# Optimization experiments

Hardware: AMD Instinct MI355X
Metric: run time of the kernel (lower is better)

## Reference

```python
import jax, jax.numpy as jnp
import numpy as np

AX = (-2, -1)
LAMBDA = 0.05
ITERS = 6

# torch fft_2d_img  = fftshift(ifft2(ifftshift(x)))  (used in the FORWARD model)
# torch ifft_2d_img = ifftshift(fft2(fftshift(x)))   (used in the ADJOINT model)

def _fwd_xform(x):
    return jnp.fft.fftshift(jnp.fft.ifft2(jnp.fft.ifftshift(x, axes=AX), axes=AX, norm='ortho'), axes=AX)

def _adj_xform(x):
    return jnp.fft.ifftshift(jnp.fft.fft2(jnp.fft.fftshift(x, axes=AX), axes=AX, norm='ortho'), axes=AX)

def _forward_model(img, S, mask):
    # img [b,t,h,w] -> masked multicoil k-space [b,t,c,h,w]
    return mask * _fwd_xform(S * img[:, :, None])

def _adjoint_model(k, S):
    # k [b,t,c,h,w] -> coil-combined image [b,t,h,w]
    return jnp.sum(jnp.conj(S) * _adj_xform(k), axis=2)

def _system_matrix_R(p, S, L, mask):
    # p [b,sv,h,w]; L [b,t,sv]
    expanded = jnp.einsum('bts,bshw->bthw', L, p)
    combined = _adjoint_model(_forward_model(expanded, S, mask), S)
    out = jnp.einsum('bts,bthw->bshw', jnp.conj(L), combined)
    return out + LAMBDA * p

def _cg_solve(b_vec, S, L, mask):
    z0 = jnp.zeros_like(b_vec)
    rs0 = jnp.vdot(b_vec, b_vec)

    def step(carry, _):
        z, r, p, rs_old, done = carry
        Ap = _system_matrix_R(p, S, L, mask)
        alpha = rs_old / (jnp.vdot(p, Ap) + 1e-20)
        z_n = z + alpha * p
        r_n = r - alpha * Ap
        rs_new = jnp.vdot(r_n, r_n)
        p_n = r_n + (rs_new / (rs_old + 1e-20)) * p
        # replicate torch early-break: freeze state once residual is tiny
        z_o = jnp.where(done, z, z_n)
        r_o = jnp.where(done, r, r_n)
        p_o = jnp.where(done, p, p_n)
        rs_o = jnp.where(done, rs_old, rs_new)
        done_n = done | (jnp.abs(rs_o) < 1e-10)
        return (z_o, r_o, p_o, rs_o, done_n), None

    carry0 = (z0, b_vec, b_vec, rs0, jnp.array(False))
    (z, _, _, _, _), _ = jax.lax.scan(step, carry0, None, length=ITERS)
    return z

def setup_inputs() -> dict:
    key = jax.random.key(0)
    ks = jax.random.split(key, 9)
    b, t, c, h, w, sv = 2, 12, 10, 256, 256, 3
    f32 = jnp.float32
    inp = {
        'k_real': jax.random.normal(ks[0], (b, t, c, h, w), f32),
        'k_imag': jax.random.normal(ks[1], (b, t, c, h, w), f32),
        'mo_real': jax.random.normal(ks[2], (b, sv, h, w), f32),
        'mo_imag': jax.random.normal(ks[3], (b, sv, h, w), f32),
        's_real': jax.random.normal(ks[4], (b, 1, c, h, w), f32),
        's_imag': jax.random.normal(ks[5], (b, 1, c, h, w), f32),
        'tb_real': jax.random.normal(ks[6], (b, t, sv), f32),
        'tb_imag': jax.random.normal(ks[7], (b, t, sv), f32),
        'mask': (jax.random.uniform(ks[8], (b, t, 1, h, w)) < 0.35).astype(f32),
    }
    return inp

def reference(k_real, k_imag, mo_real, mo_imag, s_real, s_imag, tb_real, tb_imag, mask):
    Y = k_real + 1j * k_imag          # [b,t,c,h,w]
    MO = mo_real + 1j * mo_imag       # [b,sv,h,w]
    S = s_real + 1j * s_imag          # [b,1,c,h,w]
    L = tb_real + 1j * tb_imag        # [b,t,sv]
    # b = L^H A^H Y + lambda * model_output
    b_vec = jnp.einsum('bts,bthw->bshw', jnp.conj(L), _adjoint_model(Y, S)) + LAMBDA * MO
    z = _cg_solve(b_vec, S, L, mask)  # [b,sv,h,w] complex
    return jnp.stack([z.real, z.imag], axis=-1)  # [b,sv,h,w,2] float32
```

## Files before the change

kernel.cpp:

```cpp
#include <hip/hip_runtime.h>
#include <math.h>

#define HW 65536
#define LAM 0.05f

struct Scal {
  double pap_re, pap_im, rs_acc, rs_old;
  int done, cnt;
};

__device__ __forceinline__ float2 cadd(float2 a, float2 b){ return make_float2(a.x+b.x, a.y+b.y); }
__device__ __forceinline__ float2 csub(float2 a, float2 b){ return make_float2(a.x-b.x, a.y-b.y); }
__device__ __forceinline__ float2 cmul(float2 a, float2 b){
  return make_float2(a.x*b.x - a.y*b.y, a.x*b.y + a.y*b.x);
}
__device__ __forceinline__ float2 cmulj(float2 a, float2 b){
  return make_float2(a.x*b.x + a.y*b.y, a.x*b.y - a.y*b.x);
}
__device__ __forceinline__ int rev4(int p){
  return ((p&3)<<6) | (((p>>2)&3)<<4) | (((p>>4)&3)<<2) | ((p>>6)&3);
}
__device__ __forceinline__ int swz(int p){ return p ^ (p>>4); }

__device__ __forceinline__ void wave_lds_sync(){
  __builtin_amdgcn_wave_barrier();
  __asm__ __volatile__("s_waitcnt lgkmcnt(0)" ::: "memory");
  __builtin_amdgcn_wave_barrier();
}

template<int SIGN>
__device__ __forceinline__ void bfly4(float2 x0, float2 x1, float2 x2, float2 x3,
                                      float2& y0, float2& y1, float2& y2, float2& y3){
  float2 a  = cadd(x0,x2), bm = csub(x0,x2);
  float2 c  = cadd(x1,x3), d  = csub(x1,x3);
  float2 jd = make_float2(-(float)SIGN*d.y, (float)SIGN*d.x);
  y0 = cadd(a,c); y2 = csub(a,c); y1 = cadd(bm,jd); y3 = csub(bm,jd);
}

template<int SIGN>
__device__ void wave_fft256w_x2(float2* bA, float2* bB, int lane){
#pragma unroll
  for (int st=0; st<4; ++st){
    const int B = 256 >> (2*st);
    const int Q = B >> 2;
    int m   = lane & (Q-1);
    int blk = lane >> (6 - 2*st);
    int p0  = blk*B + m;
    int i0 = swz(p0), i1 = swz(p0+Q), i2 = swz(p0+2*Q), i3 = swz(p0+3*Q);
    float2 xA0=bA[i0], xA1=bA[i1], xA2=bA[i2], xA3=bA[i3];
    float2 xB0=bB[i0], xB1=bB[i1], xB2=bB[i2], xB3=bB[i3];
    float2 yA0,yA1,yA2,yA3, yB0,yB1,yB2,yB3;
    bfly4<SIGN>(xA0,xA1,xA2,xA3, yA0,yA1,yA2,yA3);
    bfly4<SIGN>(xB0,xB1,xB2,xB3, yB0,yB1,yB2,yB3);
    if (st < 3){
      float ang = (float)SIGN * 6.28318530717958647f * (float)m / (float)B;
      float s1, c1;
      __sincosf(ang, &s1, &c1);
      float2 w1 = make_float2(c1, s1);
      float2 w2 = make_float2(c1*c1 - s1*s1, 2.f*c1*s1);
      float2 w3 = cmul(w1, w2);
      bA[i0]=yA0; bA[i1]=cmul(yA1,w1); bA[i2]=cmul(yA2,w2); bA[i3]=cmul(yA3,w3);
      bB[i0]=yB0; bB[i1]=cmul(yB1,w1); bB[i2]=cmul(yB2,w2); bB[i3]=cmul(yB3,w3);
    } else {
      int r0=swz(rev4(4*lane+0)), r1=swz(rev4(4*lane+1));
      int r2=swz(rev4(4*lane+2)), r3=swz(rev4(4*lane+3));
      bA[r0]=yA0; bA[r1]=yA1; bA[r2]=yA2; bA[r3]=yA3;
      bB[r0]=yB0; bB[r1]=yB1; bB[r2]=yB2; bB[r3]=yB3;
    }
    wave_lds_sync();
  }
}

__global__ __launch_bounds__(256) void k_w(const float* __restrict__ mask,
                                           const float* __restrict__ tbr,
                                           const float* __restrict__ tbi,
                                           float2* __restrict__ Wb,
                                           Scal* sc){
  if (blockIdx.x==0 && blockIdx.y==0 && threadIdx.x==0){
    sc->pap_re=0.0; sc->pap_im=0.0; sc->rs_acc=0.0; sc->rs_old=0.0;
    sc->done=0; sc->cnt=0;
  }
  __shared__ float2 wt[9][16][17];
  int tid = threadIdx.x;
  int bx = blockIdx.x;
  int b  = blockIdx.y;
  int u0 = (bx>>4)<<4, v0 = (bx&15)<<4;
  int u_l = tid>>4, v_l = tid&15;
  int pix = (u0+u_l)*256 + (v0+v_l);
  float d0=0,d1=0,d2=0, o01r=0,o01i=0, o02r=0,o02i=0, o12r=0,o12i=0;
#pragma unroll
  for (int t=0;t<12;t++){
    float m = mask[(size_t)(b*12+t)*HW + pix];
    int lb = (b*12+t)*3;
    float l0r = tbr[lb+0], l0i = tbi[lb+0];
    float l1r = tbr[lb+1], l1i = tbi[lb+1];
    float l2r = tbr[lb+2], l2i = tbi[lb+2];
    d0 += m*(l0r*l0r + l0i*l0i);
    d1 += m*(l1r*l1r + l1i*l1i);
    d2 += m*(l2r*l2r + l2i*l2i);
    o01r += m*(l0r*l1r + l0i*l1i); o01i += m*(l0r*l1i - l0i*l1r);
    o02r += m*(l0r*l2r + l0i*l2i); o02i += m*(l0r*l2i - l0i*l2r);
    o12r += m*(l1r*l2r + l1i*l2i); o12i += m*(l1r*l2i - l1i*l2r);
  }
  const float s = 1.0f/65536.0f;
  wt[0][u_l][v_l] = make_float2(d0*s, 0.f);
  wt[1][u_l][v_l] = make_float2(o01r*s,  o01i*s);
  wt[2][u_l][v_l] = make_float2(o02r*s,  o02i*s);
  wt[3][u_l][v_l] = make_float2(o01r*s, -o01i*s);
  wt[4][u_l][v_l] = make_float2(d1*s, 0.f);
  wt[5][u_l][v_l] = make_float2(o12r*s,  o12i*s);
  wt[6][u_l][v_l] = make_float2(o02r*s, -o02i*s);
  wt[7][u_l][v_l] = make_float2(o12r*s, -o12i*s);
  wt[8][u_l][v_l] = make_float2(d2*s, 0.f);
  __syncthreads();
  int u_l2 = tid&15, v_l2 = tid>>4;
#pragma unroll
  for (int k=0;k<9;k++){
    Wb[ ((size_t)(b*9+k)*256 + (v0+v_l2))*256 + (u0+u_l2) ] = wt[k][u_l2][v_l2];
  }
}

__global__ __launch_bounds__(256) void k_yhat(const float* __restrict__ kr,
                                              const float* __restrict__ ki,
                                              const float* __restrict__ tbr,
                                              const float* __restrict__ tbi,
                                              float2* __restrict__ bufA){
  int tid = threadIdx.x;
  int pix = (blockIdx.x*256 + tid)*4;
  int c = blockIdx.y, b = blockIdx.z;
  float ar[3][4], ai[3][4];
#pragma unroll
  for (int s=0;s<3;s++)
#pragma unroll
    for (int j=0;j<4;j++){ ar[s][j]=0.f; ai[s][j]=0.f; }
#pragma unroll
  for (int t=0;t<12;t++){
    size_t off = ((size_t)((b*12+t)*10+c))*HW + pix;
    float4 yr = *(const float4*)(kr+off);
    float4 yi = *(const float4*)(ki+off);
    float yrv[4] = {yr.x, yr.y, yr.z, yr.w};
    float yiv[4] = {yi.x, yi.y, yi.z, yi.w};
    int lb = (b*12+t)*3;
#pragma unroll
    for (int s=0;s<3;s++){
      float lr = tbr[lb+s], li = tbi[lb+s];
#pragma unroll
      for (int j=0;j<4;j++){
        ar[s][j] += lr*yrv[j] + li*yiv[j];
        ai[s][j] += lr*yiv[j] - li*yrv[j];
      }
    }
  }
  float sg0 = (((pix>>8) ^ pix) & 1) ? -1.f : 1.f;
  float sg[4] = { sg0*(1.f/256.f), -sg0*(1.f/256.f), sg0*(1.f/256.f), -sg0*(1.f/256.f) };
  size_t base = ((size_t)(b*10+c))*3*HW + pix;
#pragma unroll
  for (int s=0;s<3;s++){
    float4 o0 = make_float4(ar[s][0]*sg[0], ai[s][0]*sg[0], ar[s][1]*sg[1], ai[s][1]*sg[1]);
    float4 o1 = make_float4(ar[s][2]*sg[2], ai[s][2]*sg[2], ar[s][3]*sg[3], ai[s][3]*sg[3]);
    *(float4*)(&bufA[base + (size_t)s*HW])     = o0;
    *(float4*)(&bufA[base + (size_t)s*HW + 2]) = o1;
  }
}

template<int MODE>
__global__ __launch_bounds__(256) void k_colpass(float2* __restrict__ bufA,
                                                 const float2* __restrict__ Wb){
  __shared__ float2 lb[24*257];
  int tid = threadIdx.x, wave = tid>>6, lane = tid&63;
  int j0 = blockIdx.x*8;
  int c = blockIdx.y, b = blockIdx.z;
  for (int s=0;s<3;s++){
    const float2* src = bufA + ((size_t)(b*30 + c*3 + s))*HW;
#pragma unroll
    for (int it=0; it<4; it++){
      int idx = it*256 + tid;
      int u = idx>>2, cp = idx&3;
      float4 v = *(const float4*)(src + u*256 + j0 + 2*cp);
      lb[(s*8+2*cp  )*257 + swz(u)] = make_float2(v.x, v.y);
      lb[(s*8+2*cp+1)*257 + swz(u)] = make_float2(v.z, v.w);
    }
  }
  __syncthreads();
  if (MODE==0){
    for (int fc=wave*2; fc<24; fc+=8)
      wave_fft256w_x2<-1>(&lb[fc*257], &lb[(fc+1)*257], lane);
  } else {
    for (int fc=wave*2; fc<24; fc+=8)
      wave_fft256w_x2<1>(&lb[fc*257], &lb[(fc+1)*257], lane);
    const float2* Wp = Wb + (size_t)b*9*HW;
#pragma unroll
    for (int cc=0; cc<2; cc++){
      int col = wave*2 + cc;
      int v = j0 + col;
#pragma unroll
      for (int it=0; it<4; it++){
        int u = lane + it*64;
        int su = swz(u);
        float2 x0 = lb[(0*8+col)*257 + su];
        float2 x1 = lb[(1*8+col)*257 + su];
        float2 x2 = lb[(2*8+col)*257 + su];
        size_t wb = (size_t)v*256 + u;
        float2 y0 = cmul(Wp[(size_t)0*HW + wb], x0);
        y0 = cadd(y0, cmul(Wp[(size_t)1*HW + wb], x1));
        y0 = cadd(y0, cmul(Wp[(size_t)2*HW + wb], x2));
        float2 y1 = cmul(Wp[(size_t)3*HW + wb], x0);
        y1 = cadd(y1, cmul(Wp[(size_t)4*HW + wb], x1));
        y1 = cadd(y1, cmul(Wp[(size_t)5*HW + wb], x2));
        float2 y2 = cmul(Wp[(size_t)6*HW + wb], x0);
        y2 = cadd(y2, cmul(Wp[(size_t)7*HW + wb], x1));
        y2 = cadd(y2, cmul(Wp[(size_t)8*HW + wb], x2));
        lb[(0*8+col)*257 + su] = y0;
        lb[(1*8+col)*257 + su] = y1;
        lb[(2*8+col)*257 + su] = y2;
      }
    }
    wave_lds_sync();
    for (int fc=wave*2; fc<24; fc+=8)
      wave_fft256w_x2<-1>(&lb[fc*257], &lb[(fc+1)*257], lane);
  }
  __syncthreads();
  for (int s=0;s<3;s++){
    float2* dst = bufA + ((size_t)(b*30 + c*3 + s))*HW;
#pragma unroll
    for (int it=0; it<4; it++){
      int idx = it*256 + tid;
      int u = idx>>2, cp = idx&3;
      float2 e0 = lb[(s*8+2*cp  )*257 + swz(u)];
      float2 e1 = lb[(s*8+2*cp+1)*257 + swz(u)];
      *(float4*)(dst + u*256 + j0 + 2*cp) = make_float4(e0.x, e0.y, e1.x, e1.y);
    }
  }
}

__global__ __launch_bounds__(256) void k_spfft(float2* __restrict__ p,
                                               const float2* __restrict__ rvec,
                                               const float* __restrict__ sr_,
                                               const float* __restrict__ si_,
                                               float2* __restrict__ bufA,
                                               Scal* sc, int first){
  __shared__ float2 lb[30*257];
  int tid = threadIdx.x, wave = tid>>6, lane = tid&63;
  int r = blockIdx.x, b = blockIdx.y;
  int k = tid;
  int done = sc->done;
  float beta = 0.f;
  if (!first) beta = (float)(sc->rs_acc / (sc->rs_old + 1e-20));
  float2 pv[3];
#pragma unroll
  for (int s=0;s<3;s++){
    size_t oi = (size_t)(b*3+s)*HW + (size_t)r*256 + k;
    if (!first && !done){
      float2 po = p[oi], rv = rvec[oi];
      float2 pn = make_float2(rv.x + beta*po.x, rv.y + beta*po.y);
      p[oi] = pn; pv[s] = pn;
    } else {
      pv[s] = p[oi];
    }
  }
  int sk = swz(k);
#pragma unroll
  for (int c=0;c<10;c++){
    size_t so = (size_t)(b*10+c)*HW + (size_t)r*256 + k;
    float2 sv = make_float2(sr_[so], si_[so]);
#pragma unroll
    for (int s=0;s<3;s++)
      lb[(c*3+s)*257 + sk] = cmul(sv, pv[s]);
  }
  __syncthreads();
  for (int pl=wave*2; pl<30; pl+=8){
    float2* lwA = &lb[pl*257];
    float2* lwB = &lb[(pl+1)*257];
    wave_fft256w_x2<1>(lwA, lwB, lane);
    float2* dA = bufA + (size_t)(b*30+pl)*HW + (size_t)r*256;
    float2* dB = bufA + (size_t)(b*30+pl+1)*HW + (size_t)r*256;
#pragma unroll
    for (int q=0;q<2;q++){
      int j = lane + 64*q;
      float2 a0 = lwA[swz(2*j)], a1 = lwA[swz(2*j+1)];
      float2 b0 = lwB[swz(2*j)], b1 = lwB[swz(2*j+1)];
      *(float4*)(dA + 2*j) = make_float4(a0.x,a0.y,a1.x,a1.y);
      *(float4*)(dB + 2*j) = make_float4(b0.x,b0.y,b1.x,b1.y);
    }
  }
  if (tid==0){
    int total = (int)(gridDim.x*gridDim.y);
    int prev = atomicAdd(&sc->cnt, 1);
    if (prev == total-1){
      sc->cnt = 0;
      if (!first && !sc->done){
        sc->rs_old = sc->rs_acc;
        if (fabs(sc->rs_old) < 1e-10) sc->done = 1;
      }
      sc->pap_re = 0.0; sc->pap_im = 0.0; sc->rs_acc = 0.0;
    }
  }
}

template<int SETUP>
__global__ __launch_bounds__(256) void k_rowcomb(const float2* __restrict__ bufA,
                                                 const float* __restrict__ sr_,
                                                 const float* __restrict__ si_,
                                                 const float* __restrict__ mor,
                                                 const float* __restrict__ moi,
                                                 const float2* __restrict__ pad,
                                                 float2* __restrict__ out,
                                                 Scal* sc){
  __shared__ float2 lb[30*257];
  __shared__ double sd[4], sd2[4];
  int tid = threadIdx.x, wave = tid>>6, lane = tid&63;
  int r = blockIdx.x, b = blockIdx.y;
  for (int pl=wave*2; pl<30; pl+=8){
    const float2* sA = bufA + (size_t)(b*30+pl)*HW + (size_t)r*256;
    const float2* sB = bufA + (size_t)(b*30+pl+1)*HW + (size_t)r*256;
    float2* lwA = &lb[pl*257];
    float2* lwB = &lb[(pl+1)*257];
#pragma unroll
    for (int q=0;q<2;q++){
      int j = lane + 64*q;
      float4 va = *(const float4*)(sA + 2*j);
      float4 vb = *(const float4*)(sB + 2*j);
      lwA[swz(2*j)] = make_float2(va.x,va.y); lwA[swz(2*j+1)] = make_float2(va.z,va.w);
      lwB[swz(2*j)] = make_float2(vb.x,vb.y); lwB[swz(2*j+1)] = make_float2(vb.z,vb.w);
    }
    wave_lds_sync();
    wave_fft256w_x2<-1>(lwA, lwB, lane);
  }
  __syncthreads();
  int k = tid, sk = swz(k);
  float2 a0 = make_float2(0,0), a1 = make_float2(0,0), a2 = make_float2(0,0);
#pragma unroll
  for (int c=0;c<10;c++){
    size_t so = (size_t)(b*10+c)*HW + (size_t)r*256 + k;
    float2 sv = make_float2(sr_[so], si_[so]);
    a0 = cadd(a0, cmulj(sv, lb[(c*3+0)*257 + sk]));
    a1 = cadd(a1, cmulj(sv, lb[(c*3+1)*257 + sk]));
    a2 = cadd(a2, cmulj(sv, lb[(c*3+2)*257 + sk]));
  }
  float2 accs[3] = {a0, a1, a2};
  double dre = 0.0, dim = 0.0;
#pragma unroll
  for (int s=0;s<3;s++){
    size_t oi = (size_t)(b*3+s)*HW + (size_t)r*256 + k;
    float2 acc = accs[s];
    if (SETUP){
      float sg = ((r ^ k) & 1) ? -1.f : 1.f;
      float sl = sg * LAM;
      acc.x += sl*mor[oi]; acc.y += sl*moi[oi];
      out[oi] = acc;
      dre += (double)acc.x*acc.x + (double)acc.y*acc.y;
    } else {
      float2 av = pad[oi];
      acc.x += LAM*av.x; acc.y += LAM*av.y;
      out[oi] = acc;
      dre += (double)av.x*acc.x + (double)av.y*acc.y;
      dim += (double)av.x*acc.y - (double)av.y*acc.x;
    }
  }
  for (int off=32; off>0; off>>=1){
    dre += __shfl_down(dre, off, 64);
    if (!SETUP) dim += __shfl_down(dim, off, 64);
  }
  if (lane==0){ sd[wave] = dre; sd2[wave] = dim; }
  __syncthreads();
  if (tid==0){
    double tre = sd[0]+sd[1]+sd[2]+sd[3];
    if (SETUP){
      atomicAdd(&sc->rs_acc, tre);
    } else {
      double tim = sd2[0]+sd2[1]+sd2[2]+sd2[3];
      atomicAdd(&sc->pap_re, tre);
      atomicAdd(&sc->pap_im, tim);
    }
  }
}

__global__ __launch_bounds__(256) void k_cginit(const float2* __restrict__ bvec,
                                                float2* __restrict__ z,
                                                float2* __restrict__ r,
                                                float2* __restrict__ p,
                                                Scal* sc){
  int i = blockIdx.x*256 + threadIdx.x;
  float2 bv = bvec[i];
  z[i] = make_float2(0.f,0.f);
  r[i] = bv; p[i] = bv;
  if (i==0){ sc->rs_old = sc->rs_acc; sc->pap_re=0.0; sc->pap_im=0.0; }
}

__global__ __launch_bounds__(256) void k_upzr(float2* __restrict__ z,
                                              float2* __restrict__ r,
                                              const float2* __restrict__ p,
                                              const float2* __restrict__ Ap,
                                              Scal* sc){
  __shared__ double sd[4];
  int tid = threadIdx.x;
  int i = blockIdx.x*256 + tid;
  int done = sc->done;
  double local = 0.0;
  if (!done){
    double dre = sc->pap_re + 1e-20, dim = sc->pap_im;
    double den = dre*dre + dim*dim;
    double rs = sc->rs_old;
    float2 alpha = make_float2((float)( rs*dre/den), (float)(-rs*dim/den));
    float2 pv = p[i], apv = Ap[i];
    float2 zv = cadd(z[i], cmul(alpha, pv));
    float2 rv = csub(r[i], cmul(alpha, apv));
    z[i] = zv; r[i] = rv;
    local = (double)rv.x*rv.x + (double)rv.y*rv.y;
  }
  for (int off=32; off>0; off>>=1) local += __shfl_down(local, off, 64);
  if ((tid&63)==0) sd[tid>>6] = local;
  __syncthreads();
  if (tid==0 && !done){
    atomicAdd(&sc->rs_acc, sd[0]+sd[1]+sd[2]+sd[3]);
  }
}

__global__ __launch_bounds__(256) void k_out(const float2* __restrict__ z,
                                             float* __restrict__ out){
  int i = blockIdx.x*256 + threadIdx.x;
  int pix = i & (HW-1);
  float sgn = (((pix>>8)^pix)&1) ? -1.f : 1.f;
  float2 zv = z[i];
  out[2*i]   = sgn*zv.x;
  out[2*i+1] = sgn*zv.y;
}

extern "C" void kernel_launch(void* const* d_in, const int* in_sizes, int n_in,
                              void* d_out, int out_size, void* d_ws, size_t ws_size,
                              hipStream_t stream){
  const float* kr   = (const float*)d_in[0];
  const float* ki   = (const float*)d_in[1];
  const float* mor  = (const float*)d_in[2];
  const float* moi  = (const float*)d_in[3];
  const float* sr   = (const float*)d_in[4];
  const float* si   = (const float*)d_in[5];
  const float* tbr  = (const float*)d_in[6];
  const float* tbi  = (const float*)d_in[7];
  const float* mask = (const float*)d_in[8];
  float* out = (float*)d_out;

  float2* ws   = (float2*)d_ws;
  float2* bufA = ws;
  float2* Wb   = ws + 3932160;
  float2* bvec = ws + 5111808;
  float2* z    = ws + 5505024;
  float2* r    = ws + 5898240;
  float2* p    = ws + 6291456;
  float2* Ap   = ws + 6684672;
  Scal*   sc   = (Scal*)(ws + 7077888);

  k_w<<<dim3(256,2),dim3(256),0,stream>>>(mask, tbr, tbi, Wb, sc);
  k_yhat<<<dim3(64,10,2),dim3(256),0,stream>>>(kr, ki, tbr, tbi, bufA);
  k_colpass<0><<<dim3(32,10,2),dim3(256),0,stream>>>(bufA, Wb);
  k_rowcomb<1><<<dim3(256,2),dim3(256),0,stream>>>(bufA, sr, si, mor, moi,
                                                   (const float2*)0, bvec, sc);
  k_cginit<<<dim3(1536),dim3(256),0,stream>>>(bvec, z, r, p, sc);
  for (int it=0; it<6; ++it){
    k_spfft<<<dim3(256,2),dim3(256),0,stream>>>(p, r, sr, si, bufA, sc, it==0 ? 1 : 0);
    k_colpass<1><<<dim3(32,10,2),dim3(256),0,stream>>>(bufA, Wb);
    k_rowcomb<0><<<dim3(256,2),dim3(256),0,stream>>>(bufA, sr, si,
                                                     (const float*)0,
                                                     (const float*)0,
                                                     p, Ap, sc);
    k_upzr<<<dim3(1536),dim3(256),0,stream>>>(z, r, p, Ap, sc);
  }
  k_out<<<dim3(1536),dim3(256),0,stream>>>(z, out);
}
```

Measured before the change: 761.3 us.

## Use radix-16 register FFT with 16 lanes per transform and reorder setup passes

Replaces the four-stage radix-4 LDS FFT, where each wave handled two columns, with a two-pass radix-16 FFT done in registers. Each 256-point transform now uses 16 lanes, so 4 transforms run per wave and blocks grow to 384 or 512 threads. This is meant to cut LDS round trips, wave barriers and twiddle sincos work, and to raise parallelism across the 30 planes. The setup path now does the time-basis projection and row FFT first, then the column FFT, then a separate coil-combine kernel. The cost is heavier register pressure per thread from the 16-element arrays, plus idle threads in some phases.

```diff
diff --git a/kernel.cpp b/kernel.cpp
--- a/kernel.cpp
+++ b/kernel.cpp
@@ -17,9 +17,6 @@
 __device__ __forceinline__ float2 cmulj(float2 a, float2 b){
   return make_float2(a.x*b.x + a.y*b.y, a.x*b.y - a.y*b.x);
 }
-__device__ __forceinline__ int rev4(int p){
-  return ((p&3)<<6) | (((p>>2)&3)<<4) | (((p>>4)&3)<<2) | ((p>>6)&3);
-}
 __device__ __forceinline__ int swz(int p){ return p ^ (p>>4); }
 
 __device__ __forceinline__ void wave_lds_sync(){
@@ -28,47 +25,64 @@
   __builtin_amdgcn_wave_barrier();
 }
 
-template<int SIGN>
+template<int S>
 __device__ __forceinline__ void bfly4(float2 x0, float2 x1, float2 x2, float2 x3,
                                       float2& y0, float2& y1, float2& y2, float2& y3){
   float2 a  = cadd(x0,x2), bm = csub(x0,x2);
   float2 c  = cadd(x1,x3), d  = csub(x1,x3);
-  float2 jd = make_float2(-(float)SIGN*d.y, (float)SIGN*d.x);
+  float2 jd = make_float2(-(float)S*d.y, (float)S*d.x);
   y0 = cadd(a,c); y2 = csub(a,c); y1 = cadd(bm,jd); y3 = csub(bm,jd);
 }
 
-template<int SIGN>
-__device__ void wave_fft256w_x2(float2* bA, float2* bB, int lane){
-#pragma unroll
-  for (int st=0; st<4; ++st){
-    const int B = 256 >> (2*st);
-    const int Q = B >> 2;
-    int m   = lane & (Q-1);
-    int blk = lane >> (6 - 2*st);
-    int p0  = blk*B + m;
-    int i0 = swz(p0), i1 = swz(p0+Q), i2 = swz(p0+2*Q), i3 = swz(p0+3*Q);
-    float2 xA0=bA[i0], xA1=bA[i1], xA2=bA[i2], xA3=bA[i3];
-    float2 xB0=bB[i0], xB1=bB[i1], xB2=bB[i2], xB3=bB[i3];
-    float2 yA0,yA1,yA2,yA3, yB0,yB1,yB2,yB3;
-    bfly4<SIGN>(xA0,xA1,xA2,xA3, yA0,yA1,yA2,yA3);
-    bfly4<SIGN>(xB0,xB1,xB2,xB3, yB0,yB1,yB2,yB3);
-    if (st < 3){
-      float ang = (float)SIGN * 6.28318530717958647f * (float)m / (float)B;
-      float s1, c1;
-      __sincosf(ang, &s1, &c1);
-      float2 w1 = make_float2(c1, s1);
-      float2 w2 = make_float2(c1*c1 - s1*s1, 2.f*c1*s1);
-      float2 w3 = cmul(w1, w2);
-      bA[i0]=yA0; bA[i1]=cmul(yA1,w1); bA[i2]=cmul(yA2,w2); bA[i3]=cmul(yA3,w3);
-      bB[i0]=yB0; bB[i1]=cmul(yB1,w1); bB[i2]=cmul(yB2,w2); bB[i3]=cmul(yB3,w3);
-    } else {
-      int r0=swz(rev4(4*lane+0)), r1=swz(rev4(4*lane+1));
-      int r2=swz(rev4(4*lane+2)), r3=swz(rev4(4*lane+3));
-      bA[r0]=yA0; bA[r1]=yA1; bA[r2]=yA2; bA[r3]=yA3;
-      bB[r0]=yB0; bB[r1]=yB1; bB[r2]=yB2; bB[r3]=yB3;
-    }
-    wave_lds_sync();
-  }
+template<int S>
+__device__ __forceinline__ void dft16(float2* a){
+  const float s_ = (float)S;
+  const float2 W1 = make_float2( 0.92387953251f,  s_*0.38268343236f);
+  const float2 W2 = make_float2( 0.70710678119f,  s_*0.70710678119f);
+  const float2 W3 = make_float2( 0.38268343236f,  s_*0.92387953251f);
+  const float2 W4_ = make_float2(0.f,              s_*1.f);
+  const float2 W6 = make_float2(-0.70710678119f,  s_*0.70710678119f);
+  const float2 W9 = make_float2(-0.92387953251f, -s_*0.38268343236f);
+  float2 t[16];
+#pragma unroll
+  for (int n0=0;n0<4;n0++){
+    float2 y0,y1,y2,y3;
+    bfly4<S>(a[n0], a[n0+4], a[n0+8], a[n0+12], y0,y1,y2,y3);
+    if (n0==1){ y1=cmul(y1,W1); y2=cmul(y2,W2); y3=cmul(y3,W3); }
+    if (n0==2){ y1=cmul(y1,W2); y2=cmul(y2,W4_); y3=cmul(y3,W6); }
+    if (n0==3){ y1=cmul(y1,W3); y2=cmul(y2,W6); y3=cmul(y3,W9); }
+    t[n0*4+0]=y0; t[n0*4+1]=y1; t[n0*4+2]=y2; t[n0*4+3]=y3;
+  }
+#pragma unroll
+  for (int k1=0;k1<4;k1++){
+    float2 y0,y1,y2,y3;
+    bfly4<S>(t[0*4+k1], t[1*4+k1], t[2*4+k1], t[3*4+k1], y0,y1,y2,y3);
+    a[k1+0]=y0; a[k1+4]=y1; a[k1+8]=y2; a[k1+12]=y3;
+  }
+}
+
+template<int S>
+__device__ void fft256_r16(float2* buf, int l){
+  float2 a[16];
+#pragma unroll
+  for (int j=0;j<16;j++) a[j] = buf[swz(l + 16*j)];
+  dft16<S>(a);
+  float ang = (float)S * 6.2831853071795865f * (float)l * (1.f/256.f);
+  float sn, cs; __sincosf(ang, &sn, &cs);
+  float2 wstep = make_float2(cs, sn);
+  float2 w = wstep;
+#pragma unroll
+  for (int k=1;k<16;k++){ a[k] = cmul(a[k], w); w = cmul(w, wstep); }
+#pragma unroll
+  for (int k=0;k<16;k++) buf[swz(16*k + l)] = a[k];
+  wave_lds_sync();
+#pragma unroll
+  for (int j=0;j<16;j++) a[j] = buf[swz(16*l + j)];
+  dft16<S>(a);
+  wave_lds_sync();
+#pragma unroll
+  for (int k=0;k<16;k++) buf[swz(l + 16*k)] = a[k];
+  wave_lds_sync();
 }
 
 __global__ __launch_bounds__(256) void k_w(const float* __restrict__ mask,
@@ -120,167 +134,191 @@
   }
 }
 
-__global__ __launch_bounds__(256) void k_yhat(const float* __restrict__ kr,
+__global__ __launch_bounds__(512) void k_yrow(const float* __restrict__ kr,
                                               const float* __restrict__ ki,
                                               const float* __restrict__ tbr,
                                               const float* __restrict__ tbi,
                                               float2* __restrict__ bufA){
-  int tid = threadIdx.x;
-  int pix = (blockIdx.x*256 + tid)*4;
-  int c = blockIdx.y, b = blockIdx.z;
-  float ar[3][4], ai[3][4];
-#pragma unroll
-  for (int s=0;s<3;s++)
-#pragma unroll
-    for (int j=0;j<4;j++){ ar[s][j]=0.f; ai[s][j]=0.f; }
-#pragma unroll
-  for (int t=0;t<12;t++){
-    size_t off = ((size_t)((b*12+t)*10+c))*HW + pix;
-    float4 yr = *(const float4*)(kr+off);
-    float4 yi = *(const float4*)(ki+off);
-    float yrv[4] = {yr.x, yr.y, yr.z, yr.w};
-    float yiv[4] = {yi.x, yi.y, yi.z, yi.w};
-    int lb = (b*12+t)*3;
-#pragma unroll
-    for (int s=0;s<3;s++){
-      float lr = tbr[lb+s], li = tbi[lb+s];
-#pragma unroll
-      for (int j=0;j<4;j++){
-        ar[s][j] += lr*yrv[j] + li*yiv[j];
-        ai[s][j] += lr*yiv[j] - li*yrv[j];
-      }
-    }
-  }
-  float sg0 = (((pix>>8) ^ pix) & 1) ? -1.f : 1.f;
-  float sg[4] = { sg0*(1.f/256.f), -sg0*(1.f/256.f), sg0*(1.f/256.f), -sg0*(1.f/256.f) };
-  size_t base = ((size_t)(b*10+c))*3*HW + pix;
-#pragma unroll
-  for (int s=0;s<3;s++){
-    float4 o0 = make_float4(ar[s][0]*sg[0], ai[s][0]*sg[0], ar[s][1]*sg[1], ai[s][1]*sg[1]);
-    float4 o1 = make_float4(ar[s][2]*sg[2], ai[s][2]*sg[2], ar[s][3]*sg[3], ai[s][3]*sg[3]);
-    *(float4*)(&bufA[base + (size_t)s*HW])     = o0;
-    *(float4*)(&bufA[base + (size_t)s*HW + 2]) = o1;
+  __shared__ float2 lb[30*257];
+  int tid = threadIdx.x;
+  int wv = tid>>6, lane = tid&63, g = lane>>4, l = lane&15;
+  int px = tid & 255, half = tid >> 8;
+  int r = blockIdx.x, b = blockIdx.y;
+  float sg = (((r ^ px) & 1) ? -1.f : 1.f) * (1.f/256.f);
+  int sk = swz(px);
+#pragma unroll
+  for (int cc=0; cc<5; cc++){
+    int c = half*5 + cc;
+    float a0r=0,a0i=0,a1r=0,a1i=0,a2r=0,a2i=0;
+#pragma unroll
+    for (int t=0;t<12;t++){
+      size_t off = ((size_t)((b*12+t)*10+c))*HW + (size_t)r*256 + px;
+      float yr = kr[off], yi = ki[off];
+      int lbi = (b*12+t)*3;
+      float l0r = tbr[lbi+0], l0i = tbi[lbi+0];
+      float l1r = tbr[lbi+1], l1i = tbi[lbi+1];
+      float l2r = tbr[lbi+2], l2i = tbi[lbi+2];
+      a0r += l0r*yr + l0i*yi;  a0i += l0r*yi - l0i*yr;
+      a1r += l1r*yr + l1i*yi;  a1i += l1r*yi - l1i*yr;
+      a2r += l2r*yr + l2i*yi;  a2i += l2r*yi - l2i*yr;
+    }
+    lb[(c*3+0)*257 + sk] = make_float2(a0r*sg, a0i*sg);
+    lb[(c*3+1)*257 + sk] = make_float2(a1r*sg, a1i*sg);
+    lb[(c*3+2)*257 + sk] = make_float2(a2r*sg, a2i*sg);
+  }
+  __syncthreads();
+  int tau = 4*wv + g;
+  if (tau < 30){
+    float2* lw = &lb[tau*257];
+    fft256_r16<-1>(lw, l);
+    float2* dst = bufA + (size_t)(b*30+tau)*HW + (size_t)r*256;
+#pragma unroll
+    for (int j=0;j<8;j++){
+      int e = 2*(16*j + l);
+      float2 e0 = lw[swz(e)], e1 = lw[swz(e+1)];
+      *(float4*)(dst + e) = make_float4(e0.x,e0.y,e1.x,e1.y);
+    }
   }
 }
 
 template<int MODE>
-__global__ __launch_bounds__(256) void k_colpass(float2* __restrict__ bufA,
+__global__ __launch_bounds__(384) void k_colpass(float2* __restrict__ bufA,
                                                  const float2* __restrict__ Wb){
   __shared__ float2 lb[24*257];
-  int tid = threadIdx.x, wave = tid>>6, lane = tid&63;
+  int tid = threadIdx.x;
+  int wv = tid>>6, lane = tid&63, g = lane>>4, l = lane&15;
   int j0 = blockIdx.x*8;
   int c = blockIdx.y, b = blockIdx.z;
-  for (int s=0;s<3;s++){
-    const float2* src = bufA + ((size_t)(b*30 + c*3 + s))*HW;
-#pragma unroll
-    for (int it=0; it<4; it++){
-      int idx = it*256 + tid;
-      int u = idx>>2, cp = idx&3;
-      float4 v = *(const float4*)(src + u*256 + j0 + 2*cp);
-      lb[(s*8+2*cp  )*257 + swz(u)] = make_float2(v.x, v.y);
-      lb[(s*8+2*cp+1)*257 + swz(u)] = make_float2(v.z, v.w);
-    }
-  }
-  __syncthreads();
+#pragma unroll
+  for (int it=0; it<8; it++){
+    int idx = it*384 + tid;
+    int s = idx>>10, rem = idx&1023, u = rem>>2, cp = rem&3;
+    const float2* src = bufA + (size_t)(b*30 + c*3 + s)*HW;
+    float4 v = *(const float4*)(src + u*256 + j0 + 2*cp);
+    lb[(s*8+2*cp  )*257 + swz(u)] = make_float2(v.x, v.y);
+    lb[(s*8+2*cp+1)*257 + swz(u)] = make_float2(v.z, v.w);
+  }
+  __syncthreads();
+  int tau = 4*wv + g;
   if (MODE==0){
-    for (int fc=wave*2; fc<24; fc+=8)
-      wave_fft256w_x2<-1>(&lb[fc*257], &lb[(fc+1)*257], lane);
+    fft256_r16<-1>(&lb[tau*257], l);
   } else {
-    for (int fc=wave*2; fc<24; fc+=8)
-      wave_fft256w_x2<1>(&lb[fc*257], &lb[(fc+1)*257], lane);
+    fft256_r16<1>(&lb[tau*257], l);
+    __syncthreads();
     const float2* Wp = Wb + (size_t)b*9*HW;
-#pragma unroll
-    for (int cc=0; cc<2; cc++){
-      int col = wave*2 + cc;
+    for (int idx=tid; idx<2048; idx+=384){
+      int u = idx&255, col = idx>>8;
+      int su = swz(u);
       int v = j0 + col;
-#pragma unroll
-      for (int it=0; it<4; it++){
-        int u = lane + it*64;
-        int su = swz(u);
-        float2 x0 = lb[(0*8+col)*257 + su];
-        float2 x1 = lb[(1*8+col)*257 + su];
-        float2 x2 = lb[(2*8+col)*257 + su];
-        size_t wb = (size_t)v*256 + u;
-        float2 y0 = cmul(Wp[(size_t)0*HW + wb], x0);
-        y0 = cadd(y0, cmul(Wp[(size_t)1*HW + wb], x1));
-        y0 = cadd(y0, cmul(Wp[(size_t)2*HW + wb], x2));
-        float2 y1 = cmul(Wp[(size_t)3*HW + wb], x0);
-        y1 = cadd(y1, cmul(Wp[(size_t)4*HW + wb], x1));
-        y1 = cadd(y1, cmul(Wp[(size_t)5*HW + wb], x2));
-        float2 y2 = cmul(Wp[(size_t)6*HW + wb], x0);
-        y2 = cadd(y2, cmul(Wp[(size_t)7*HW + wb], x1));
-        y2 = cadd(y2, cmul(Wp[(size_t)8*HW + wb], x2));
-        lb[(0*8+col)*257 + su] = y0;
-        lb[(1*8+col)*257 + su] = y1;
-        lb[(2*8+col)*257 + su] = y2;
-      }
-    }
-    wave_lds_sync();
-    for (int fc=wave*2; fc<24; fc+=8)
-      wave_fft256w_x2<-1>(&lb[fc*257], &lb[(fc+1)*257], lane);
-  }
-  __syncthreads();
-  for (int s=0;s<3;s++){
-    float2* dst = bufA + ((size_t)(b*30 + c*3 + s))*HW;
-#pragma unroll
-    for (int it=0; it<4; it++){
-      int idx = it*256 + tid;
-      int u = idx>>2, cp = idx&3;
-      float2 e0 = lb[(s*8+2*cp  )*257 + swz(u)];
-      float2 e1 = lb[(s*8+2*cp+1)*257 + swz(u)];
-      *(float4*)(dst + u*256 + j0 + 2*cp) = make_float4(e0.x, e0.y, e1.x, e1.y);
-    }
-  }
-}
-
-__global__ __launch_bounds__(256) void k_spfft(float2* __restrict__ p,
+      float2 x0 = lb[(0*8+col)*257 + su];
+      float2 x1 = lb[(1*8+col)*257 + su];
+      float2 x2 = lb[(2*8+col)*257 + su];
+      size_t wb = (size_t)v*256 + u;
+      float2 y0 = cmul(Wp[(size_t)0*HW + wb], x0);
+      y0 = cadd(y0, cmul(Wp[(size_t)1*HW + wb], x1));
+      y0 = cadd(y0, cmul(Wp[(size_t)2*HW + wb], x2));
+      float2 y1 = cmul(Wp[(size_t)3*HW + wb], x0);
+      y1 = cadd(y1, cmul(Wp[(size_t)4*HW + wb], x1));
+      y1 = cadd(y1, cmul(Wp[(size_t)5*HW + wb], x2));
+      float2 y2 = cmul(Wp[(size_t)6*HW + wb], x0);
+      y2 = cadd(y2, cmul(Wp[(size_t)7*HW + wb], x1));
+      y2 = cadd(y2, cmul(Wp[(size_t)8*HW + wb], x2));
+      lb[(0*8+col)*257 + su] = y0;
+      lb[(1*8+col)*257 + su] = y1;
+      lb[(2*8+col)*257 + su] = y2;
+    }
+    __syncthreads();
+    fft256_r16<-1>(&lb[tau*257], l);
+  }
+  __syncthreads();
+#pragma unroll
+  for (int it=0; it<8; it++){
+    int idx = it*384 + tid;
+    int s = idx>>10, rem = idx&1023, u = rem>>2, cp = rem&3;
+    float2* dst = bufA + (size_t)(b*30 + c*3 + s)*HW;
+    float2 e0 = lb[(s*8+2*cp  )*257 + swz(u)];
+    float2 e1 = lb[(s*8+2*cp+1)*257 + swz(u)];
+    *(float4*)(dst + u*256 + j0 + 2*cp) = make_float4(e0.x, e0.y, e1.x, e1.y);
+  }
+}
+
+__global__ __launch_bounds__(256) void k_combine(const float2* __restrict__ bufA,
+                                                 const float* __restrict__ sr_,
+                                                 const float* __restrict__ si_,
+                                                 const float* __restrict__ mor,
+                                                 const float* __restrict__ moi,
+                                                 float2* __restrict__ bvec,
+                                                 Scal* sc){
+  __shared__ double sd[4];
+  int tid = threadIdx.x;
+  int i = blockIdx.x*256 + tid;
+  int pix = i & (HW-1);
+  int bs = i >> 16;
+  int b = bs/3, s = bs - 3*b;
+  float2 acc = make_float2(0.f, 0.f);
+#pragma unroll
+  for (int c=0;c<10;c++){
+    float2 F  = bufA[(size_t)(b*30 + c*3 + s)*HW + pix];
+    size_t so = (size_t)(b*10+c)*HW + pix;
+    float2 sv = make_float2(sr_[so], si_[so]);
+    acc = cadd(acc, cmulj(sv, F));
+  }
+  float sgl = (((pix>>8)^pix)&1 ? -1.f : 1.f) * LAM;
+  acc.x += sgl*mor[i]; acc.y += sgl*moi[i];
+  bvec[i] = acc;
+  double dre = (double)acc.x*acc.x + (double)acc.y*acc.y;
+  for (int off=32; off>0; off>>=1) dre += __shfl_down(dre, off, 64);
+  if ((tid&63)==0) sd[tid>>6] = dre;
+  __syncthreads();
+  if (tid==0) atomicAdd(&sc->rs_acc, sd[0]+sd[1]+sd[2]+sd[3]);
+}
+
+__global__ __launch_bounds__(512) void k_spfft(float2* __restrict__ p,
                                                const float2* __restrict__ rvec,
                                                const float* __restrict__ sr_,
                                                const float* __restrict__ si_,
                                                float2* __restrict__ bufA,
                                                Scal* sc, int first){
   __shared__ float2 lb[30*257];
-  int tid = threadIdx.x, wave = tid>>6, lane = tid&63;
+  int tid = threadIdx.x;
+  int wv = tid>>6, lane = tid&63, g = lane>>4, l = lane&15;
   int r = blockIdx.x, b = blockIdx.y;
-  int k = tid;
-  int done = sc->done;
-  float beta = 0.f;
-  if (!first) beta = (float)(sc->rs_acc / (sc->rs_old + 1e-20));
-  float2 pv[3];
-#pragma unroll
-  for (int s=0;s<3;s++){
-    size_t oi = (size_t)(b*3+s)*HW + (size_t)r*256 + k;
-    if (!first && !done){
-      float2 po = p[oi], rv = rvec[oi];
-      float2 pn = make_float2(rv.x + beta*po.x, rv.y + beta*po.y);
-      p[oi] = pn; pv[s] = pn;
-    } else {
-      pv[s] = p[oi];
-    }
-  }
-  int sk = swz(k);
-#pragma unroll
-  for (int c=0;c<10;c++){
-    size_t so = (size_t)(b*10+c)*HW + (size_t)r*256 + k;
-    float2 sv = make_float2(sr_[so], si_[so]);
-#pragma unroll
-    for (int s=0;s<3;s++)
-      lb[(c*3+s)*257 + sk] = cmul(sv, pv[s]);
-  }
-  __syncthreads();
-  for (int pl=wave*2; pl<30; pl+=8){
-    float2* lwA = &lb[pl*257];
-    float2* lwB = &lb[(pl+1)*257];
-    wave_fft256w_x2<1>(lwA, lwB, lane);
-    float2* dA = bufA + (size_t)(b*30+pl)*HW + (size_t)r*256;
-    float2* dB = bufA + (size_t)(b*30+pl+1)*HW + (size_t)r*256;
-#pragma unroll
-    for (int q=0;q<2;q++){
-      int j = lane + 64*q;
-      float2 a0 = lwA[swz(2*j)], a1 = lwA[swz(2*j+1)];
-      float2 b0 = lwB[swz(2*j)], b1 = lwB[swz(2*j+1)];
-      *(float4*)(dA + 2*j) = make_float4(a0.x,a0.y,a1.x,a1.y);
-      *(float4*)(dB + 2*j) = make_float4(b0.x,b0.y,b1.x,b1.y);
+  if (tid < 256){
+    int px = tid, sk = swz(px);
+    int done = sc->done;
+    float beta = first ? 0.f : (float)(sc->rs_acc / (sc->rs_old + 1e-20));
+    float2 pv[3];
+#pragma unroll
+    for (int s=0;s<3;s++){
+      size_t oi = (size_t)(b*3+s)*HW + (size_t)r*256 + px;
+      if (!first && !done){
+        float2 po = p[oi], rv = rvec[oi];
+        float2 pn = make_float2(rv.x + beta*po.x, rv.y + beta*po.y);
+        p[oi] = pn; pv[s] = pn;
+      } else {
+        pv[s] = p[oi];
+      }
+    }
+#pragma unroll
+    for (int c=0;c<10;c++){
+      size_t so = (size_t)(b*10+c)*HW + (size_t)r*256 + px;
+      float2 sv = make_float2(sr_[so], si_[so]);
+      lb[(c*3+0)*257 + sk] = cmul(sv, pv[0]);
+      lb[(c*3+1)*257 + sk] = cmul(sv, pv[1]);
+      lb[(c*3+2)*257 + sk] = cmul(sv, pv[2]);
+    }
+  }
+  __syncthreads();
+  int tau = 4*wv + g;
+  if (tau < 30){
+    float2* lw = &lb[tau*257];
+    fft256_r16<1>(lw, l);
+    float2* dst = bufA + (size_t)(b*30+tau)*HW + (size_t)r*256;
+#pragma unroll
+    for (int j=0;j<8;j++){
+      int e = 2*(16*j + l);
+      float2 e0 = lw[swz(e)], e1 = lw[swz(e+1)];
+      *(float4*)(dst + e) = make_float4(e0.x,e0.y,e1.x,e1.y);
     }
   }
   if (tid==0){
@@ -297,81 +335,68 @@
   }
 }
 
-template<int SETUP>
-__global__ __launch_bounds__(256) void k_rowcomb(const float2* __restrict__ bufA,
+__global__ __launch_bounds__(512) void k_rowcomb(const float2* __restrict__ bufA,
                                                  const float* __restrict__ sr_,
                                                  const float* __restrict__ si_,
-                                                 const float* __restrict__ mor,
-                                                 const float* __restrict__ moi,
-                                                 const float2* __restrict__ pad,
-                                                 float2* __restrict__ out,
+                                                 const float2* __restrict__ pvec,
+                                                 float2* __restrict__ Ap,
                                                  Scal* sc){
   __shared__ float2 lb[30*257];
-  __shared__ double sd[4], sd2[4];
-  int tid = threadIdx.x, wave = tid>>6, lane = tid&63;
+  __shared__ double sd[8], sd2[8];
+  int tid = threadIdx.x;
+  int wv = tid>>6, lane = tid&63, g = lane>>4, l = lane&15;
   int r = blockIdx.x, b = blockIdx.y;
-  for (int pl=wave*2; pl<30; pl+=8){
-    const float2* sA = bufA + (size_t)(b*30+pl)*HW + (size_t)r*256;
-    const float2* sB = bufA + (size_t)(b*30+pl+1)*HW + (size_t)r*256;
-    float2* lwA = &lb[pl*257];
-    float2* lwB = &lb[(pl+1)*257];
-#pragma unroll
-    for (int q=0;q<2;q++){
-      int j = lane + 64*q;
-      float4 va = *(const float4*)(sA + 2*j);
-      float4 vb = *(const float4*)(sB + 2*j);
-      lwA[swz(2*j)] = make_float2(va.x,va.y); lwA[swz(2*j+1)] = make_float2(va.z,va.w);
-      lwB[swz(2*j)] = make_float2(vb.x,vb.y); lwB[swz(2*j+1)] = make_float2(vb.z,vb.w);
+  int tau = 4*wv + g;
+  if (tau < 30){
+    const float2* src = bufA + (size_t)(b*30+tau)*HW + (size_t)r*256;
+    float2* lw = &lb[tau*257];
+#pragma unroll
+    for (int j=0;j<8;j++){
+      int e = 2*(16*j + l);
+      float4 v = *(const float4*)(src + e);
+      lw[swz(e)]   = make_float2(v.x, v.y);
+      lw[swz(e+1)] = make_float2(v.z, v.w);
     }
     wave_lds_sync();
-    wave_fft256w_x2<-1>(lwA, lwB, lane);
-  }
-  __syncthreads();
-  int k = tid, sk = swz(k);
-  float2 a0 = make_float2(0,0), a1 = make_float2(0,0), a2 = make_float2(0,0);
-#pragma unroll
-  for (int c=0;c<10;c++){
-    size_t so = (size_t)(b*10+c)*HW + (size_t)r*256 + k;
-    float2 sv = make_float2(sr_[so], si_[so]);
-    a0 = cadd(a0, cmulj(sv, lb[(c*3+0)*257 + sk]));
-    a1 = cadd(a1, cmulj(sv, lb[(c*3+1)*257 + sk]));
-    a2 = cadd(a2, cmulj(sv, lb[(c*3+2)*257 + sk]));
-  }
-  float2 accs[3] = {a0, a1, a2};
+    fft256_r16<-1>(lw, l);
+  }
+  __syncthreads();
   double dre = 0.0, dim = 0.0;
-#pragma unroll
-  for (int s=0;s<3;s++){
-    size_t oi = (size_t)(b*3+s)*HW + (size_t)r*256 + k;
-    float2 acc = accs[s];
-    if (SETUP){
-      float sg = ((r ^ k) & 1) ? -1.f : 1.f;
-      float sl = sg * LAM;
-      acc.x += sl*mor[oi]; acc.y += sl*moi[oi];
-      out[oi] = acc;
-      dre += (double)acc.x*acc.x + (double)acc.y*acc.y;
-    } else {
-      float2 av = pad[oi];
+  if (tid < 256){
+    int px = tid, sk = swz(px);
+    float2 a0={0,0}, a1={0,0}, a2={0,0};
+#pragma unroll
+    for (int c=0;c<10;c++){
+      size_t so = (size_t)(b*10+c)*HW + (size_t)r*256 + px;
+      float2 sv = make_float2(sr_[so], si_[so]);
+      a0 = cadd(a0, cmulj(sv, lb[(c*3+0)*257 + sk]));
+      a1 = cadd(a1, cmulj(sv, lb[(c*3+1)*257 + sk]));
+      a2 = cadd(a2, cmulj(sv, lb[(c*3+2)*257 + sk]));
+    }
+    float2 accs[3] = {a0,a1,a2};
+#pragma unroll
+    for (int s=0;s<3;s++){
+      size_t oi = (size_t)(b*3+s)*HW + (size_t)r*256 + px;
+      float2 acc = accs[s];
+      float2 av = pvec[oi];
       acc.x += LAM*av.x; acc.y += LAM*av.y;
-      out[oi] = acc;
+      Ap[oi] = acc;
       dre += (double)av.x*acc.x + (double)av.y*acc.y;
       dim += (double)av.x*acc.y - (double)av.y*acc.x;
     }
   }
   for (int off=32; off>0; off>>=1){
     dre += __shfl_down(dre, off, 64);
-    if (!SETUP) dim += __shfl_down(dim, off, 64);
-  }
-  if (lane==0){ sd[wave] = dre; sd2[wave] = dim; }
+    dim += __shfl_down(dim, off, 64);
+  }
+  if (lane==0){ sd[wv]=dre; sd2[wv]=dim; }
   __syncthreads();
   if (tid==0){
-    double tre = sd[0]+sd[1]+sd[2]+sd[3];
-    if (SETUP){
-      atomicAdd(&sc->rs_acc, tre);
-    } else {
-      double tim = sd2[0]+sd2[1]+sd2[2]+sd2[3];
-      atomicAdd(&sc->pap_re, tre);
-      atomicAdd(&sc->pap_im, tim);
-    }
+    double tre=0.0, tim=0.0;
+#pragma unroll
+    for (int q=0;q<8;q++){ tre+=sd[q]; tim+=sd2[q]; }
+    atomicAdd(&sc->pap_re, tre);
+    atomicAdd(&sc->pap_im, tim);
   }
 }
 
@@ -451,18 +476,14 @@
   Scal*   sc   = (Scal*)(ws + 7077888);
 
   k_w<<<dim3(256,2),dim3(256),0,stream>>>(mask, tbr, tbi, Wb, sc);
-  k_yhat<<<dim3(64,10,2),dim3(256),0,stream>>>(kr, ki, tbr, tbi, bufA);
-  k_colpass<0><<<dim3(32,10,2),dim3(256),0,stream>>>(bufA, Wb);
-  k_rowcomb<1><<<dim3(256,2),dim3(256),0,stream>>>(bufA, sr, si, mor, moi,
-                                                   (const float2*)0, bvec, sc);
+  k_yrow<<<dim3(256,2),dim3(512),0,stream>>>(kr, ki, tbr, tbi, bufA);
+  k_colpass<0><<<dim3(32,10,2),dim3(384),0,stream>>>(bufA, Wb);
+  k_combine<<<dim3(1536),dim3(256),0,stream>>>(bufA, sr, si, mor, moi, bvec, sc);
   k_cginit<<<dim3(1536),dim3(256),0,stream>>>(bvec, z, r, p, sc);
   for (int it=0; it<6; ++it){
-    k_spfft<<<dim3(256,2),dim3(256),0,stream>>>(p, r, sr, si, bufA, sc, it==0 ? 1 : 0);
-    k_colpass<1><<<dim3(32,10,2),dim3(256),0,stream>>>(bufA, Wb);
-    k_rowcomb<0><<<dim3(256,2),dim3(256),0,stream>>>(bufA, sr, si,
-                                                     (const float*)0,
-                                                     (const float*)0,
-                                                     p, Ap, sc);
+    k_spfft<<<dim3(256,2),dim3(512),0,stream>>>(p, r, sr, si, bufA, sc, it==0 ? 1 : 0);
+    k_colpass<1><<<dim3(32,10,2),dim3(384),0,stream>>>(bufA, Wb);
+    k_rowcomb<<<dim3(256,2),dim3(512),0,stream>>>(bufA, sr, si, p, Ap, sc);
     k_upzr<<<dim3(1536),dim3(256),0,stream>>>(z, r, p, Ap, sc);
   }
   k_out<<<dim3(1536),dim3(256),0,stream>>>(z, out);
```

Result: no change. 750.3 us (-1.4%).
